# Optimization experiments

Hardware: AMD Instinct MI355X
Metric: run time of the kernel (lower is better)

The kernel has to match this reference:

```python
import jax, jax.numpy as jnp
import numpy as np

C = 32        # channels after first 1x1 conv
HEADS = 4     # FuncSelfAttention heads ('channel' head split -> d = C // HEADS)


def setup_inputs() -> dict:
    key = jax.random.key(0)
    ks = jax.random.split(key, 8)
    B, H, W = 8, 512, 512
    s = 0.1
    return {
        "x": jax.random.normal(ks[0], (B, 1, H, W), jnp.float32),
        "n": 8,
        "m": 8,
        # Conv2d(1, C, kernel_size=1) == per-pixel linear 1->C
        "w1": jax.random.normal(ks[1], (C, 1), jnp.float32) * s,
        "b1": jax.random.normal(ks[2], (C,), jnp.float32) * s,
        # fused QKV projection over channels, bias=False
        "wqkv": jax.random.normal(ks[3], (3 * C, C), jnp.float32) * s,
        # output projection of the attention
        "wproj": jax.random.normal(ks[4], (C, C), jnp.float32) * s,
        "bproj": jax.random.normal(ks[5], (C,), jnp.float32) * s,
        # Conv2d(C, 1, kernel_size=1)
        "w2": jax.random.normal(ks[6], (1, C), jnp.float32) * s,
        "b2": jax.random.normal(ks[7], (1,), jnp.float32) * s,
    }


def reference(x, n, m, w1, b1, wqkv, wproj, bproj, w2, b2):
    B, _, H, W = x.shape
    d = C // HEADS
    hh, ww = H // n, W // m
    S, P = n * m, hh * ww  # subdomain tokens, quadrature points per token

    # 1x1 conv (pointwise linear over channel dim)
    h = jnp.einsum('oi,bihw->bohw', w1, x) + b1[None, :, None, None]

    # decompose2d: [B,C,H,W] -> [B, n*m, C, hh, ww] (flatten spatial per token)
    u = h.reshape(B, C, n, hh, m, ww).transpose(0, 2, 4, 1, 3, 5)
    u = u.reshape(B, S, C, P)

    # channel self-attention over subdomain functions
    qkv = jnp.einsum('oc,bscp->bsop', wqkv, u)          # [B,S,3C,P]
    q, k, v = jnp.split(qkv, 3, axis=2)
    q = q.reshape(B, S, HEADS, d, P)
    k = k.reshape(B, S, HEADS, d, P)
    v = v.reshape(B, S, HEADS, d, P)

    # L2 (quadrature-mean) inner product over points + head channels
    scale = 1.0 / (P * np.sqrt(d).astype(np.float32))
    scores = jnp.einsum('bihdp,bjhdp->bhij', q, k) * scale  # [B,H,S,S]
    attn = jax.nn.softmax(scores, axis=-1)
    o = jnp.einsum('bhij,bjhdp->bihdp', attn, v).reshape(B, S, C, P)
    o = jnp.einsum('oc,bscp->bsop', wproj, o) + bproj[None, None, :, None]

    # recompose2d: [B, n*m, C, hh, ww] -> [B, C, H, W]
    o = o.reshape(B, n, m, C, hh, ww).transpose(0, 3, 1, 4, 2, 5)
    o = o.reshape(B, C, H, W)

    # final 1x1 conv C -> 1
    out = jnp.einsum('oc,bchw->bohw', w2, o) + b2[None, :, None, None]
    return out
```

## Files before the change

### kernel.cpp

```cpp
#include <hip/hip_runtime.h>


#define CONST_OFF 0
#define SXP_OFF   16
#define WB_OFF    (16 + 256*64)
#define PART_OFF  (WB_OFF + 8*2048)

typedef __attribute__((ext_vector_type(8))) short bf16x8;
typedef __attribute__((ext_vector_type(4))) float f32x4;

__device__ __forceinline__ unsigned short f2bf(float f) {
    unsigned int u = __float_as_uint(f);
    u = (u + 0x7FFFu + ((u >> 16) & 1u)) >> 16;
    return (unsigned short)u;
}

__global__ __launch_bounds__(256) void k1_gram(const float* __restrict__ x,
                                               float* __restrict__ ws)
{
    __shared__ unsigned short xsb[64 * 136];
    int b = blockIdx.x >> 5, prg2 = blockIdx.x & 31;
    int t = threadIdx.x;
    const float* xb = x + (size_t)b * 262144;

    float4 v[8];
    #pragma unroll
    for (int u = 0; u < 8; ++u) {
        int q = t + 256 * u;
        int prl = q >> 10, rem = q & 1023;
        int tj = rem >> 7, col4 = rem & 127;
        v[u] = *(const float4*)(xb + (tj * 64 + prg2 * 2 + prl) * 512 + col4 * 4);
    }
    #pragma unroll
    for (int u = 0; u < 8; ++u) {
        int q = t + 256 * u;
        int prl = q >> 10, rem = q & 1023;
        int tj = rem >> 7, col4 = rem & 127;
        int token = tj * 8 + (col4 >> 4);
        ushort4 h;
        h.x = f2bf(v[u].x); h.y = f2bf(v[u].y); h.z = f2bf(v[u].z); h.w = f2bf(v[u].w);
        *(ushort4*)(&xsb[token * 136 + prl * 64 + (col4 & 15) * 4]) = h;
    }
    __syncthreads();

    if (t < 64) {
        const uint4* p = (const uint4*)(&xsb[t * 136]);
        float s = 0.f;
        #pragma unroll
        for (int c = 0; c < 16; ++c) {
            uint4 u = p[c];
            s += __uint_as_float(u.x << 16) + __uint_as_float(u.x & 0xFFFF0000u)
               + __uint_as_float(u.y << 16) + __uint_as_float(u.y & 0xFFFF0000u)
               + __uint_as_float(u.z << 16) + __uint_as_float(u.z & 0xFFFF0000u)
               + __uint_as_float(u.w << 16) + __uint_as_float(u.w & 0xFFFF0000u);
        }
        ws[SXP_OFF + blockIdx.x * 64 + t] = s;
    }

    int w = t >> 6, lane = t & 63;
    int m = lane & 15, quad = lane >> 4;
    f32x4 acc[4];
    #pragma unroll
    for (int jq = 0; jq < 4; ++jq) acc[jq] = (f32x4){0.f, 0.f, 0.f, 0.f};

    #pragma unroll
    for (int s = 0; s < 4; ++s) {
        int kb = s * 32 + quad * 8;
        bf16x8 a = *(const bf16x8*)(&xsb[(w * 16 + m) * 136 + kb]);
        #pragma unroll
        for (int jq = 0; jq < 4; ++jq) {
            bf16x8 bb = *(const bf16x8*)(&xsb[(jq * 16 + m) * 136 + kb]);
            acc[jq] = __builtin_amdgcn_mfma_f32_16x16x32_bf16(a, bb, acc[jq],
                                                              0, 0, 0);
        }
    }

    float* part = ws + PART_OFF + (size_t)blockIdx.x * 4096;
    #pragma unroll
    for (int jq = 0; jq < 4; ++jq)
        #pragma unroll
        for (int r = 0; r < 4; ++r)
            part[(w * 16 + quad * 4 + r) * 64 + jq * 16 + m] = acc[jq][r];
}

__global__ __launch_bounds__(256) void k2_attn(
    const float* __restrict__ w1, const float* __restrict__ b1,
    const float* __restrict__ wqkv, const float* __restrict__ wproj,
    const float* __restrict__ bproj, const float* __restrict__ w2,
    const float* __restrict__ b2, float* __restrict__ ws)
{
    __shared__ float arow[96], crow[96], pvec[32];
    __shared__ float cst[16];
    __shared__ float G_s[8 * 65];
    __shared__ float sxp_s[4][64];
    __shared__ float sx_s[64];
    __shared__ float coef_s[4][8];
    __shared__ float m_s[4][8];
    int b = blockIdx.x >> 3, rg = blockIdx.x & 7;
    int t = threadIdx.x;

    if (t < 96) {
        float sa = 0.f, sc = 0.f;
        for (int c = 0; c < 32; ++c) {
            float w = wqkv[t * 32 + c];
            sa += w * w1[c];
            sc += w * b1[c];
        }
        arow[t] = sa; crow[t] = sc;
    } else if (t < 128) {
        int c = t - 96;
        float s = 0.f;
        for (int oc = 0; oc < 32; ++oc) s += w2[oc] * wproj[oc * 32 + c];
        pvec[c] = s;
    }

    {
        const float* p0 = ws + PART_OFF + (size_t)(b * 32) * 4096 + rg * 512;
        float a0 = 0.f, a1 = 0.f;
        #pragma unroll
        for (int r = 0; r < 32; ++r) {
            const float* pr = p0 + (size_t)r * 4096;
            a0 += pr[t]; a1 += pr[t + 256];
        }
        int e0 = t;          G_s[(e0 >> 6) * 65 + (e0 & 63)] = a0;
        int e1 = t + 256;    G_s[(e1 >> 6) * 65 + (e1 & 63)] = a1;
    }

    {
        int j = t & 63, r4 = t >> 6;
        float s = 0.f;
        #pragma unroll
        for (int k = 0; k < 8; ++k)
            s += ws[SXP_OFF + (b * 32 + r4 * 8 + k) * 64 + j];
        sxp_s[r4][j] = s;
    }
    __syncthreads();
    if (t < 64)
        sx_s[t] = sxp_s[0][t] + sxp_s[1][t] + sxp_s[2][t] + sxp_s[3][t];

    const float scale = 1.0f / (4096.0f * 2.8284271247461903f);
    if (t >= 64 && t < 68) {
        int h = t - 64;
        float A = 0.f, Bk = 0.f, g = 0.f;
        #pragma unroll
        for (int dd = 0; dd < 8; ++dd) {
            int o = h * 8 + dd;
            A  += arow[o] * arow[32 + o];
            Bk += crow[o] * arow[32 + o];
            g  += pvec[o] * arow[64 + o];
        }
        cst[h]     = A * scale;
        cst[4 + h] = Bk * scale;
        cst[8 + h] = g;
    } else if (t == 68) {
        float c0 = b2[0];
        for (int c = 0; c < 32; ++c)  c0 += pvec[c] * crow[64 + c];
        for (int oc = 0; oc < 32; ++oc) c0 += w2[oc] * bproj[oc];
        cst[12] = c0;
    }
    __syncthreads();

    {
        int pair = t >> 3, jg = t & 7;
        int h = pair >> 3, il = pair & 7;
        float A  = cst[h];
        float Bk = cst[4 + h];
        float sv[8];
        float mloc = -1e30f;
        #pragma unroll
        for (int jj = 0; jj < 8; ++jj) {
            int j = jg * 8 + jj;
            float s = A * G_s[il * 65 + j] + Bk * sx_s[j];
            sv[jj] = s;
            mloc = fmaxf(mloc, s);
        }
        mloc = fmaxf(mloc, __shfl_xor(mloc, 1));
        mloc = fmaxf(mloc, __shfl_xor(mloc, 2));
        mloc = fmaxf(mloc, __shfl_xor(mloc, 4));
        float z = 0.f;
        #pragma unroll
        for (int jj = 0; jj < 8; ++jj) z += __expf(sv[jj] - mloc);
        z += __shfl_xor(z, 1);
        z += __shfl_xor(z, 2);
        z += __shfl_xor(z, 4);
        if (jg == 0) {
            coef_s[h][il] = cst[8 + h] / z;
            m_s[h][il]    = mloc;
        }
    }
    __syncthreads();

    {
        float A0 = cst[0], A1 = cst[1], A2 = cst[2], A3 = cst[3];
        float B0 = cst[4], B1 = cst[5], B2 = cst[6], B3 = cst[7];
        unsigned short* wout =
            (unsigned short*)(ws + WB_OFF) + b * 4096 + rg * 512;
        #pragma unroll
        for (int k = 0; k < 2; ++k) {
            int e = t + 256 * k;
            int il = e >> 6, j = e & 63;
            float G  = G_s[il * 65 + j];
            float sx = sx_s[j];
            float w =
                coef_s[0][il] * __expf(A0 * G + B0 * sx - m_s[0][il]) +
                coef_s[1][il] * __expf(A1 * G + B1 * sx - m_s[1][il]) +
                coef_s[2][il] * __expf(A2 * G + B2 * sx - m_s[2][il]) +
                coef_s[3][il] * __expf(A3 * G + B3 * sx - m_s[3][il]);
            wout[e] = f2bf(w);
        }
    }
    if (b == 0 && rg == 0 && t == 68) ws[CONST_OFF + 12] = cst[12];
}

__global__ __launch_bounds__(256) void k3_apply(const float* __restrict__ x,
                                                const float* __restrict__ ws,
                                                float* __restrict__ out)
{
    __shared__ unsigned short xt[64 * 72];
    __shared__ unsigned short wsm[64 * 72];
    int b = blockIdx.x >> 6, pr = blockIdx.x & 63;
    int t = threadIdx.x;
    const float* xb = x + (size_t)b * 262144;

    const uint4* wb = (const uint4*)((const unsigned short*)(ws + WB_OFF)
                                     + b * 4096);
    uint4 wv[2];
    #pragma unroll
    for (int k = 0; k < 2; ++k) wv[k] = wb[t + 256 * k];

    float4 v[4];
    #pragma unroll
    for (int k = 0; k < 4; ++k) {
        int q = t + 256 * k;
        int j = q >> 4, c4 = q & 15;
        int ti = j >> 3, tk = j & 7;
        v[k] = *(const float4*)(xb + (ti * 64 + pr) * 512 + tk * 64 + c4 * 4);
    }

    #pragma unroll
    for (int k = 0; k < 4; ++k) {
        int q = t + 256 * k;
        int j = q >> 4, c4 = q & 15;
        int jx = j ^ ((c4 & 7) << 3);
        xt[(4 * c4 + 0) * 72 + jx] = f2bf(v[k].x);
        xt[(4 * c4 + 1) * 72 + jx] = f2bf(v[k].y);
        xt[(4 * c4 + 2) * 72 + jx] = f2bf(v[k].z);
        xt[(4 * c4 + 3) * 72 + jx] = f2bf(v[k].w);
    }
    {
        #pragma unroll
        for (int k = 0; k < 2; ++k) {
            int q = t + 256 * k;
            int i = q >> 3, j8 = q & 7;
            *(uint4*)(&wsm[i * 72 + j8 * 8]) = wv[k];
        }
    }
    __syncthreads();

    int w = t >> 6, lane = t & 63;
    int m = lane & 15, quad = lane >> 4;
    f32x4 acc[4];
    #pragma unroll
    for (int jq = 0; jq < 4; ++jq) acc[jq] = (f32x4){0.f, 0.f, 0.f, 0.f};

    #pragma unroll
    for (int s = 0; s < 2; ++s) {
        int kb = s * 32 + quad * 8;
        bf16x8 a = *(const bf16x8*)(&wsm[(w * 16 + m) * 72 + kb]);
        #pragma unroll
        for (int jq = 0; jq < 4; ++jq) {
            int row = jq * 16 + m;
            int kbx = kb ^ (((row >> 2) & 7) << 3);
            bf16x8 bv = *(const bf16x8*)(&xt[row * 72 + kbx]);
            acc[jq] = __builtin_amdgcn_mfma_f32_16x16x32_bf16(a, bv, acc[jq],
                                                              0, 0, 0);
        }
    }

    float c0 = ws[CONST_OFF + 12];
    float* ob = out + (size_t)b * 262144;
    #pragma unroll
    for (int jq = 0; jq < 4; ++jq)
        #pragma unroll
        for (int r = 0; r < 4; ++r) {
            int i = w * 16 + quad * 4 + r;
            int c = jq * 16 + m;
            int ti = i >> 3, tk = i & 7;
            ob[(ti * 64 + pr) * 512 + tk * 64 + c] = acc[jq][r] + c0;
        }
}

extern "C" void kernel_launch(void* const* d_in, const int* in_sizes, int n_in,
                              void* d_out, int out_size, void* d_ws, size_t ws_size,
                              hipStream_t stream) {
    const float* x     = (const float*)d_in[0];
    const float* w1    = (const float*)d_in[3];
    const float* b1    = (const float*)d_in[4];
    const float* wqkv  = (const float*)d_in[5];
    const float* wproj = (const float*)d_in[6];
    const float* bproj = (const float*)d_in[7];
    const float* w2    = (const float*)d_in[8];
    const float* b2    = (const float*)d_in[9];
    float* out = (float*)d_out;
    float* ws  = (float*)d_ws;

    k1_gram<<<256, 256, 0, stream>>>(x, ws);
    k2_attn<<<64, 256, 0, stream>>>(w1, b1, wqkv, wproj, bproj, w2, b2, ws);
    k3_apply<<<512, 256, 0, stream>>>(x, ws, out);
}
```

Before: 88.79 us.

## Fuse gram and attention kernels via cooperative launch with grid sync

```diff
diff --git a/kernel.cpp b/kernel.cpp
--- a/kernel.cpp
+++ b/kernel.cpp
@@ -1,4 +1,7 @@
 #include <hip/hip_runtime.h>
+#include <hip/hip_cooperative_groups.h>
+
+namespace cg = cooperative_groups;
 
 
 #define CONST_OFF 0
@@ -15,11 +18,24 @@
     return (unsigned short)u;
 }
 
-__global__ __launch_bounds__(256) void k1_gram(const float* __restrict__ x,
-                                               float* __restrict__ ws)
+__global__ __launch_bounds__(256) void k12_gram_attn(
+    const float* __restrict__ x,
+    const float* __restrict__ w1, const float* __restrict__ b1,
+    const float* __restrict__ wqkv, const float* __restrict__ wproj,
+    const float* __restrict__ bproj, const float* __restrict__ w2,
+    const float* __restrict__ b2, float* __restrict__ ws)
 {
     __shared__ unsigned short xsb[64 * 136];
-    int b = blockIdx.x >> 5, prg2 = blockIdx.x & 31;
+    __shared__ float arow[96], crow[96], pvec[32];
+    __shared__ float cst[16];
+    __shared__ float G_s[8 * 65];
+    __shared__ float sxp_s[4][64];
+    __shared__ float sx_s[64];
+    __shared__ float coef_s[4][8];
+    __shared__ float m_s[4][8];
+
+    int bid = blockIdx.x;
+    int b = bid >> 5, prg2 = bid & 31;
     int t = threadIdx.x;
     const float* xb = x + (size_t)b * 262144;
 
@@ -54,50 +70,43 @@
                + __uint_as_float(u.z << 16) + __uint_as_float(u.z & 0xFFFF0000u)
                + __uint_as_float(u.w << 16) + __uint_as_float(u.w & 0xFFFF0000u);
         }
-        ws[SXP_OFF + blockIdx.x * 64 + t] = s;
-    }
-
-    int w = t >> 6, lane = t & 63;
-    int m = lane & 15, quad = lane >> 4;
-    f32x4 acc[4];
-    #pragma unroll
-    for (int jq = 0; jq < 4; ++jq) acc[jq] = (f32x4){0.f, 0.f, 0.f, 0.f};
-
-    #pragma unroll
-    for (int s = 0; s < 4; ++s) {
-        int kb = s * 32 + quad * 8;
-        bf16x8 a = *(const bf16x8*)(&xsb[(w * 16 + m) * 136 + kb]);
-        #pragma unroll
-        for (int jq = 0; jq < 4; ++jq) {
-            bf16x8 bb = *(const bf16x8*)(&xsb[(jq * 16 + m) * 136 + kb]);
-            acc[jq] = __builtin_amdgcn_mfma_f32_16x16x32_bf16(a, bb, acc[jq],
-                                                              0, 0, 0);
-        }
-    }
-
-    float* part = ws + PART_OFF + (size_t)blockIdx.x * 4096;
-    #pragma unroll
-    for (int jq = 0; jq < 4; ++jq)
-        #pragma unroll
-        for (int r = 0; r < 4; ++r)
-            part[(w * 16 + quad * 4 + r) * 64 + jq * 16 + m] = acc[jq][r];
-}
-
-__global__ __launch_bounds__(256) void k2_attn(
-    const float* __restrict__ w1, const float* __restrict__ b1,
-    const float* __restrict__ wqkv, const float* __restrict__ wproj,
-    const float* __restrict__ bproj, const float* __restrict__ w2,
-    const float* __restrict__ b2, float* __restrict__ ws)
-{
-    __shared__ float arow[96], crow[96], pvec[32];
-    __shared__ float cst[16];
-    __shared__ float G_s[8 * 65];
-    __shared__ float sxp_s[4][64];
-    __shared__ float sx_s[64];
-    __shared__ float coef_s[4][8];
-    __shared__ float m_s[4][8];
-    int b = blockIdx.x >> 3, rg = blockIdx.x & 7;
-    int t = threadIdx.x;
+        ws[SXP_OFF + bid * 64 + t] = s;
+    }
+
+    {
+        int w = t >> 6, lane = t & 63;
+        int m = lane & 15, quad = lane >> 4;
+        f32x4 acc[4];
+        #pragma unroll
+        for (int jq = 0; jq < 4; ++jq) acc[jq] = (f32x4){0.f, 0.f, 0.f, 0.f};
+
+        #pragma unroll
+        for (int s = 0; s < 4; ++s) {
+            int kb = s * 32 + quad * 8;
+            bf16x8 a = *(const bf16x8*)(&xsb[(w * 16 + m) * 136 + kb]);
+            #pragma unroll
+            for (int jq = 0; jq < 4; ++jq) {
+                bf16x8 bb = *(const bf16x8*)(&xsb[(jq * 16 + m) * 136 + kb]);
+                acc[jq] = __builtin_amdgcn_mfma_f32_16x16x32_bf16(a, bb, acc[jq],
+                                                                  0, 0, 0);
+            }
+        }
+
+        float* part = ws + PART_OFF + (size_t)bid * 4096;
+        #pragma unroll
+        for (int jq = 0; jq < 4; ++jq)
+            #pragma unroll
+            for (int r = 0; r < 4; ++r)
+                part[(w * 16 + quad * 4 + r) * 64 + jq * 16 + m] = acc[jq][r];
+    }
+
+    __threadfence();
+    cg::this_grid().sync();
+
+    if (bid >= 64) return;
+    __threadfence();
+
+    int bq = bid >> 3, rg = bid & 7;
 
     if (t < 96) {
         float sa = 0.f, sc = 0.f;
@@ -115,7 +124,7 @@
     }
 
     {
-        const float* p0 = ws + PART_OFF + (size_t)(b * 32) * 4096 + rg * 512;
+        const float* p0 = ws + PART_OFF + (size_t)(bq * 32) * 4096 + rg * 512;
         float a0 = 0.f, a1 = 0.f;
         #pragma unroll
         for (int r = 0; r < 32; ++r) {
@@ -131,7 +140,7 @@
         float s = 0.f;
         #pragma unroll
         for (int k = 0; k < 8; ++k)
-            s += ws[SXP_OFF + (b * 32 + r4 * 8 + k) * 64 + j];
+            s += ws[SXP_OFF + (bq * 32 + r4 * 8 + k) * 64 + j];
         sxp_s[r4][j] = s;
     }
     __syncthreads();
@@ -153,10 +162,10 @@
         cst[4 + h] = Bk * scale;
         cst[8 + h] = g;
     } else if (t == 68) {
-        float c0 = b2[0];
-        for (int c = 0; c < 32; ++c)  c0 += pvec[c] * crow[64 + c];
-        for (int oc = 0; oc < 32; ++oc) c0 += w2[oc] * bproj[oc];
-        cst[12] = c0;
+        float c0v = b2[0];
+        for (int c = 0; c < 32; ++c)  c0v += pvec[c] * crow[64 + c];
+        for (int oc = 0; oc < 32; ++oc) c0v += w2[oc] * bproj[oc];
+        cst[12] = c0v;
     }
     __syncthreads();
 
@@ -194,7 +203,7 @@
         float A0 = cst[0], A1 = cst[1], A2 = cst[2], A3 = cst[3];
         float B0 = cst[4], B1 = cst[5], B2 = cst[6], B3 = cst[7];
         unsigned short* wout =
-            (unsigned short*)(ws + WB_OFF) + b * 4096 + rg * 512;
+            (unsigned short*)(ws + WB_OFF) + bq * 4096 + rg * 512;
         #pragma unroll
         for (int k = 0; k < 2; ++k) {
             int e = t + 256 * k;
@@ -209,7 +218,7 @@
             wout[e] = f2bf(w);
         }
     }
-    if (b == 0 && rg == 0 && t == 68) ws[CONST_OFF + 12] = cst[12];
+    if (bid == 0 && t == 68) ws[CONST_OFF + 12] = cst[12];
 }
 
 __global__ __launch_bounds__(256) void k3_apply(const float* __restrict__ x,
@@ -304,7 +313,10 @@
     float* out = (float*)d_out;
     float* ws  = (float*)d_ws;
 
-    k1_gram<<<256, 256, 0, stream>>>(x, ws);
-    k2_attn<<<64, 256, 0, stream>>>(w1, b1, wqkv, wproj, bproj, w2, b2, ws);
+    void* args[] = {(void*)&x, (void*)&w1, (void*)&b1, (void*)&wqkv,
+                    (void*)&wproj, (void*)&bproj, (void*)&w2, (void*)&b2,
+                    (void*)&ws};
+    (void)hipLaunchCooperativeKernel((const void*)k12_gram_attn, dim3(256),
+                                     dim3(256), args, 0, stream);
     k3_apply<<<512, 256, 0, stream>>>(x, ws, out);
 }
```

Measured after the change: 185.4 us. 2.09x slower.
